# Kernel tuning notes

Hardware: AMD Instinct MI355X
Metric: run time of the kernel (lower is better)

The kernel has to match this reference:

```python
import jax, jax.numpy as jnp
import numpy as np

NUM_LAYERS = 3


def setup_inputs() -> dict:
    key = jax.random.key(0)
    k1, k2 = jax.random.split(key)
    N = 200000          # num_users + num_items
    D = 64              # latent_dim
    E = 4000000         # number of directed edges
    edge_index = jax.random.randint(k1, (2, E), 0, N, dtype=jnp.int64)
    emb_weight = 0.1 * jax.random.normal(k2, (N, D), dtype=jnp.float32)  # nn.init.normal_(std=0.1)
    return {"edge_index": edge_index, "emb_weight": emb_weight}


def reference(edge_index, emb_weight):
    N, D = emb_weight.shape
    src, dst = edge_index[0], edge_index[1]
    # gcn_norm (no self loops), as used by LGConv
    deg = jax.ops.segment_sum(jnp.ones_like(src, dtype=emb_weight.dtype), dst, num_segments=N)
    dinv = jnp.where(deg > 0, jax.lax.rsqrt(jnp.maximum(deg, 1.0)), 0.0)
    norm = dinv[src] * dinv[dst]            # [E]
    emb0 = emb_weight
    emb = emb0
    acc = emb0                              # running sum over layer embeddings
    for _ in range(NUM_LAYERS):
        msgs = norm[:, None] * emb[src]     # [E, D] irregular gather
        emb = jax.ops.segment_sum(msgs, dst, num_segments=N)  # scatter-add aggregate
        acc = acc + emb
    out = acc / (NUM_LAYERS + 1)            # mean over stacked layer embeddings
    return (emb0, out)
```

## Files before the change

### kernel.cpp

```cpp
#include <hip/hip_runtime.h>

#define DIM 64
#define BNODE_SHIFT 9
#define BNODE (1 << BNODE_SHIFT)
#define MAXNB 512
#define BIN_CHUNK 8192

__device__ inline float bf2f(unsigned int h) {
    return __uint_as_float((h & 0xFFFFu) << 16);
}
__device__ inline unsigned int f2bf2(float a, float b) {
    unsigned int ua = __float_as_uint(a);
    unsigned int ub = __float_as_uint(b);
    ua = (ua + 0x7FFFu + ((ua >> 16) & 1u)) >> 16;
    ub = (ub + 0x7FFFu + ((ub >> 16) & 1u)) >> 16;
    return ua | (ub << 16);
}

__global__ void hist_kernel(const int* __restrict__ dst, int* __restrict__ bucket_count,
                            int E, int NB) {
    __shared__ int h[MAXNB];
    const int t = threadIdx.x;
    for (int i = t; i < MAXNB; i += blockDim.x) h[i] = 0;
    __syncthreads();
    const long long beg = (long long)blockIdx.x * BIN_CHUNK;
    for (int j = 0; j < BIN_CHUNK / 256; ++j) {
        long long idx = beg + j * 256 + t;
        if (idx < E) atomicAdd(&h[dst[idx] >> BNODE_SHIFT], 1);
    }
    __syncthreads();
    for (int b = t; b < NB; b += blockDim.x)
        if (h[b]) atomicAdd(&bucket_count[b], h[b]);
}

__global__ void __launch_bounds__(MAXNB) bucket_scan_kernel(
        const int* __restrict__ bucket_count, int* __restrict__ bucket_base,
        int* __restrict__ bucket_cursor, int NB) {
    __shared__ int s[MAXNB];
    const int t = threadIdx.x;
    int c = (t < NB) ? bucket_count[t] : 0;
    s[t] = c;
    __syncthreads();
    for (int off = 1; off < MAXNB; off <<= 1) {
        int v = s[t];
        int a = (t >= off) ? s[t - off] : 0;
        __syncthreads();
        s[t] = v + a;
        __syncthreads();
    }
    if (t < NB) {
        int excl = s[t] - c;
        bucket_base[t] = excl;
        bucket_cursor[t] = excl;
    }
    if (t == 0) bucket_base[NB] = s[MAXNB - 1];
}

__global__ void bin_kernel(const int* __restrict__ src, const int* __restrict__ dst,
                           int* __restrict__ bucket_cursor, unsigned int* __restrict__ packed,
                           int E, int NB) {
    __shared__ int lhist[MAXNB];
    __shared__ int lbase[MAXNB];
    const int t = threadIdx.x;
    for (int i = t; i < MAXNB; i += blockDim.x) lhist[i] = 0;
    __syncthreads();
    const long long beg = (long long)blockIdx.x * BIN_CHUNK;
    for (int j = 0; j < BIN_CHUNK / 256; ++j) {
        long long idx = beg + j * 256 + t;
        if (idx < E) atomicAdd(&lhist[dst[idx] >> BNODE_SHIFT], 1);
    }
    __syncthreads();
    for (int b = t; b < NB; b += blockDim.x) {
        int c = lhist[b];
        lbase[b] = c ? atomicAdd(&bucket_cursor[b], c) : 0;
    }
    __syncthreads();
    for (int i = t; i < MAXNB; i += blockDim.x) lhist[i] = 0;
    __syncthreads();
    for (int j = 0; j < BIN_CHUNK / 256; ++j) {
        long long idx = beg + j * 256 + t;
        if (idx < E) {
            int d = dst[idx];
            int b = d >> BNODE_SHIFT;
            int lpos = atomicAdd(&lhist[b], 1);
            packed[lbase[b] + lpos] =
                (unsigned int)src[idx] | ((unsigned int)(d & (BNODE - 1)) << 18);
        }
    }
}

__global__ void __launch_bounds__(BNODE) csr_kernel(
        const int* __restrict__ bucket_base, const unsigned int* __restrict__ packed,
        int* __restrict__ csr_src, float* __restrict__ dinv,
        int4* __restrict__ desc, int N) {
    __shared__ int hist[BNODE];
    __shared__ int s[BNODE];
    const int t = threadIdx.x;
    const int b = blockIdx.x;
    const int b0 = bucket_base[b];
    const int cnt = bucket_base[b + 1] - b0;
    hist[t] = 0;
    __syncthreads();
    for (int i = t; i < cnt; i += BNODE)
        atomicAdd(&hist[packed[b0 + i] >> 18], 1);
    __syncthreads();
    s[t] = hist[t];
    __syncthreads();
    for (int off = 1; off < BNODE; off <<= 1) {
        int v = s[t];
        int a = (t >= off) ? s[t - off] : 0;
        __syncthreads();
        s[t] = v + a;
        __syncthreads();
    }
    const int deg = hist[t];
    const int excl = s[t] - deg;
    const int myBeg = b0 + excl;
    const int node = (b << BNODE_SHIFT) + t;
    float di2 = 0.0f;
    if (node < N) {
        float fd = (float)deg;
        di2 = deg > 0 ? 1.0f / fd : 0.0f;
        dinv[node] = deg > 0 ? rsqrtf(fd) : 0.0f;
    }
    __syncthreads();
    s[t] = excl;
    __syncthreads();
    for (int i = t; i < cnt; i += BNODE) {
        unsigned int p = packed[b0 + i];
        int lpos = atomicAdd(&s[p >> 18], 1);
        csr_src[b0 + lpos] = (int)(p & 0x3FFFFu);
    }
    __syncthreads();
    const int bin = deg < (BNODE - 1) ? deg : (BNODE - 1);
    hist[t] = 0;
    __syncthreads();
    atomicAdd(&hist[bin], 1);
    __syncthreads();
    s[t] = hist[t];
    __syncthreads();
    for (int off = 1; off < BNODE; off <<= 1) {
        int v = s[t];
        int a = (t >= off) ? s[t - off] : 0;
        __syncthreads();
        s[t] = v + a;
        __syncthreads();
    }
    int tot = hist[t];
    __syncthreads();
    hist[t] = s[t] - tot;
    __syncthreads();
    int pos = atomicAdd(&hist[bin], 1);
    desc[(b << BNODE_SHIFT) + pos] =
        make_int4(myBeg, myBeg + deg, node < N ? node : 0x7FFFFFFF, __float_as_int(di2));
}

__global__ void conv0_kernel(const float* __restrict__ emb0, const float* __restrict__ dinv,
                             float* __restrict__ out_emb0, unsigned int* __restrict__ S0,
                             int n4) {
    int i = blockIdx.x * blockDim.x + threadIdx.x;
    if (i >= n4) return;
    float4 v = ((const float4*)emb0)[i];
    ((float4*)out_emb0)[i] = v;
    float w = dinv[i >> 4];
    uint2 o;
    o.x = f2bf2(w * v.x, w * v.y);
    o.y = f2bf2(w * v.z, w * v.w);
    ((uint2*)S0)[i] = o;
}

template<bool LAST>
__global__ void gather_kernel(const int4* __restrict__ desc,
                              const int* __restrict__ csr_src,
                              const unsigned int* __restrict__ S_in,
                              unsigned int* __restrict__ S_out,
                              const unsigned int* __restrict__ S1,
                              const float* __restrict__ emb0,
                              float* __restrict__ acc,
                              int N, int NG) {
    int tid = blockIdx.x * blockDim.x + threadIdx.x;
    int g = tid >> 3;
    int q = tid & 7;
    if (g >= NG) return;
    const int4 d = desc[g];
    const int node = d.z;
    if (node >= N) return;
    float r0 = 0.f, r1 = 0.f, r2 = 0.f, r3 = 0.f, r4 = 0.f, r5 = 0.f, r6 = 0.f, r7 = 0.f;
    for (int i = d.x; i < d.y; ++i) {
        int sIdx = csr_src[i];
        uint4 gg = *(const uint4*)(S_in + (size_t)sIdx * (DIM / 2) + q * 4);
        r0 += bf2f(gg.x);
        r1 += bf2f(gg.x >> 16);
        r2 += bf2f(gg.y);
        r3 += bf2f(gg.y >> 16);
        r4 += bf2f(gg.z);
        r5 += bf2f(gg.z >> 16);
        r6 += bf2f(gg.w);
        r7 += bf2f(gg.w >> 16);
    }
    const float di2 = __int_as_float(d.w);
    if (!LAST) {
        uint4 o;
        o.x = f2bf2(di2 * r0, di2 * r1);
        o.y = f2bf2(di2 * r2, di2 * r3);
        o.z = f2bf2(di2 * r4, di2 * r5);
        o.w = f2bf2(di2 * r6, di2 * r7);
        *(uint4*)(S_out + (size_t)node * (DIM / 2) + q * 4) = o;
    } else {
        float rs = di2 > 0.f ? rsqrtf(di2) : 0.f;
        float dv = sqrtf(di2);
        uint4 a1 = *(const uint4*)(S1   + (size_t)node * (DIM / 2) + q * 4);
        uint4 a2 = *(const uint4*)(S_in + (size_t)node * (DIM / 2) + q * 4);
        const float* e = emb0 + (size_t)node * DIM + q * 8;
        float4 e0 = *(const float4*)(e);
        float4 e1 = *(const float4*)(e + 4);
        float4 o0, o1;
        o0.x = 0.25f * (e0.x + rs * (bf2f(a1.x) + bf2f(a2.x)) + dv * r0);
        o0.y = 0.25f * (e0.y + rs * (bf2f(a1.x >> 16) + bf2f(a2.x >> 16)) + dv * r1);
        o0.z = 0.25f * (e0.z + rs * (bf2f(a1.y) + bf2f(a2.y)) + dv * r2);
        o0.w = 0.25f * (e0.w + rs * (bf2f(a1.y >> 16) + bf2f(a2.y >> 16)) + dv * r3);
        o1.x = 0.25f * (e1.x + rs * (bf2f(a1.z) + bf2f(a2.z)) + dv * r4);
        o1.y = 0.25f * (e1.y + rs * (bf2f(a1.z >> 16) + bf2f(a2.z >> 16)) + dv * r5);
        o1.z = 0.25f * (e1.z + rs * (bf2f(a1.w) + bf2f(a2.w)) + dv * r6);
        o1.w = 0.25f * (e1.w + rs * (bf2f(a1.w >> 16) + bf2f(a2.w >> 16)) + dv * r7);
        float* ap = acc + (size_t)node * DIM + q * 8;
        *(float4*)(ap) = o0;
        *(float4*)(ap + 4) = o1;
    }
}

static inline size_t align256(size_t x) { return (x + 255) & ~(size_t)255; }

extern "C" void kernel_launch(void* const* d_in, const int* in_sizes, int n_in,
                              void* d_out, int out_size, void* d_ws, size_t ws_size,
                              hipStream_t stream) {
    const int*   edge = (const int*)d_in[0];
    const float* emb0 = (const float*)d_in[1];
    const int E = in_sizes[0] / 2;
    const int N = in_sizes[1] / DIM;
    const int* src = edge;
    const int* dst = edge + E;
    const int NB = (N + BNODE - 1) >> BNODE_SHIFT;

    char* ws = (char*)d_ws;
    int* bucket_count  = (int*)ws;  ws += align256((size_t)(MAXNB + 1) * sizeof(int));
    int* bucket_base   = (int*)ws;  ws += align256((size_t)(MAXNB + 1) * sizeof(int));
    int* bucket_cursor = (int*)ws;  ws += align256((size_t)(MAXNB + 1) * sizeof(int));
    float* dinv        = (float*)ws; ws += align256((size_t)N * sizeof(float));
    int4* desc         = (int4*)ws; ws += align256((size_t)NB * BNODE * sizeof(int4));
    unsigned int* packed = (unsigned int*)ws; ws += align256((size_t)E * sizeof(int));
    int* csr_src       = (int*)ws;  ws += align256((size_t)E * sizeof(int));
    unsigned int* SX   = (unsigned int*)ws; ws += align256((size_t)N * (DIM / 2) * sizeof(unsigned int));
    unsigned int* SY   = (unsigned int*)ws; ws += align256((size_t)N * (DIM / 2) * sizeof(unsigned int));

    float* out_emb0 = (float*)d_out;
    float* acc      = out_emb0 + (size_t)N * DIM;

    const int blocks_e = (int)(((long long)E + BIN_CHUNK - 1) / BIN_CHUNK);
    const int n4 = N * DIM / 4;

    hipMemsetAsync(bucket_count, 0, (size_t)(MAXNB + 1) * sizeof(int), stream);
    hist_kernel<<<blocks_e, 256, 0, stream>>>(dst, bucket_count, E, NB);
    bucket_scan_kernel<<<1, MAXNB, 0, stream>>>(bucket_count, bucket_base, bucket_cursor, NB);
    bin_kernel<<<blocks_e, 256, 0, stream>>>(src, dst, bucket_cursor, packed, E, NB);
    csr_kernel<<<NB, BNODE, 0, stream>>>(bucket_base, packed, csr_src, dinv, desc, N);

    conv0_kernel<<<(n4 + 255) / 256, 256, 0, stream>>>(emb0, dinv, out_emb0, SX, n4);

    const int NG = NB * BNODE;
    const int ggrid = (NG * 8 + 255) / 256;
    gather_kernel<false><<<ggrid, 256, 0, stream>>>(desc, csr_src, SX, SY, nullptr, nullptr, nullptr, N, NG);
    gather_kernel<false><<<ggrid, 256, 0, stream>>>(desc, csr_src, SY, SX, nullptr, nullptr, nullptr, N, NG);
    gather_kernel<true><<<ggrid, 256, 0, stream>>>(desc, csr_src, SX, nullptr, SY, emb0, acc, N, NG);
}
```

Before: 608.1 us.

## Assign one wavefront per node in gather and drop degree-sorted descriptors

The gather kernels now map each node to a 64-lane wavefront. Eight edge groups of eight lanes each read rows in parallel, with two loads in flight per lane, and the partial sums are combined with xor shuffles. The degree-binning sort of node descriptors in the CSR kernel is removed, so descriptors are written directly by node index. This is meant to expose more memory-level parallelism per node and remove the load imbalance of one 8-lane group walking a whole edge list. The cost is eight times as many threads and shuffle-reduction overhead for low-degree nodes, where most lanes sit idle.

```diff
diff --git a/kernel.cpp b/kernel.cpp
--- a/kernel.cpp
+++ b/kernel.cpp
@@ -117,11 +117,11 @@
     const int excl = s[t] - deg;
     const int myBeg = b0 + excl;
     const int node = (b << BNODE_SHIFT) + t;
-    float di2 = 0.0f;
     if (node < N) {
         float fd = (float)deg;
-        di2 = deg > 0 ? 1.0f / fd : 0.0f;
+        float di2 = deg > 0 ? 1.0f / fd : 0.0f;
         dinv[node] = deg > 0 ? rsqrtf(fd) : 0.0f;
+        desc[node] = make_int4(myBeg, myBeg + deg, deg, __float_as_int(di2));
     }
     __syncthreads();
     s[t] = excl;
@@ -131,28 +131,6 @@
         int lpos = atomicAdd(&s[p >> 18], 1);
         csr_src[b0 + lpos] = (int)(p & 0x3FFFFu);
     }
-    __syncthreads();
-    const int bin = deg < (BNODE - 1) ? deg : (BNODE - 1);
-    hist[t] = 0;
-    __syncthreads();
-    atomicAdd(&hist[bin], 1);
-    __syncthreads();
-    s[t] = hist[t];
-    __syncthreads();
-    for (int off = 1; off < BNODE; off <<= 1) {
-        int v = s[t];
-        int a = (t >= off) ? s[t - off] : 0;
-        __syncthreads();
-        s[t] = v + a;
-        __syncthreads();
-    }
-    int tot = hist[t];
-    __syncthreads();
-    hist[t] = s[t] - tot;
-    __syncthreads();
-    int pos = atomicAdd(&hist[bin], 1);
-    desc[(b << BNODE_SHIFT) + pos] =
-        make_int4(myBeg, myBeg + deg, node < N ? node : 0x7FFFFFFF, __float_as_int(di2));
 }
 
 __global__ void conv0_kernel(const float* __restrict__ emb0, const float* __restrict__ dinv,
@@ -169,6 +147,13 @@
     ((uint2*)S0)[i] = o;
 }
 
+__device__ inline void acc8(float r[8], uint4 g) {
+    r[0] += bf2f(g.x); r[1] += bf2f(g.x >> 16);
+    r[2] += bf2f(g.y); r[3] += bf2f(g.y >> 16);
+    r[4] += bf2f(g.z); r[5] += bf2f(g.z >> 16);
+    r[6] += bf2f(g.w); r[7] += bf2f(g.w >> 16);
+}
+
 template<bool LAST>
 __global__ void gather_kernel(const int4* __restrict__ desc,
                               const int* __restrict__ csr_src,
@@ -177,53 +162,61 @@
                               const unsigned int* __restrict__ S1,
                               const float* __restrict__ emb0,
                               float* __restrict__ acc,
-                              int N, int NG) {
-    int tid = blockIdx.x * blockDim.x + threadIdx.x;
-    int g = tid >> 3;
-    int q = tid & 7;
-    if (g >= NG) return;
-    const int4 d = desc[g];
-    const int node = d.z;
+                              int N) {
+    const int node = (blockIdx.x * blockDim.x + threadIdx.x) >> 6;
     if (node >= N) return;
-    float r0 = 0.f, r1 = 0.f, r2 = 0.f, r3 = 0.f, r4 = 0.f, r5 = 0.f, r6 = 0.f, r7 = 0.f;
-    for (int i = d.x; i < d.y; ++i) {
-        int sIdx = csr_src[i];
-        uint4 gg = *(const uint4*)(S_in + (size_t)sIdx * (DIM / 2) + q * 4);
-        r0 += bf2f(gg.x);
-        r1 += bf2f(gg.x >> 16);
-        r2 += bf2f(gg.y);
-        r3 += bf2f(gg.y >> 16);
-        r4 += bf2f(gg.z);
-        r5 += bf2f(gg.z >> 16);
-        r6 += bf2f(gg.w);
-        r7 += bf2f(gg.w >> 16);
-    }
+    const int lane = threadIdx.x & 63;
+    const int eg = lane >> 3;
+    const int q  = lane & 7;
+    const int4 d = desc[node];
+    const int end = d.y;
+    float r[8] = {0.f, 0.f, 0.f, 0.f, 0.f, 0.f, 0.f, 0.f};
+    int i = d.x + eg;
+    for (; i + 8 < end; i += 16) {
+        int s0 = csr_src[i];
+        int s1 = csr_src[i + 8];
+        uint4 g0 = *(const uint4*)(S_in + (size_t)s0 * (DIM / 2) + q * 4);
+        uint4 g1 = *(const uint4*)(S_in + (size_t)s1 * (DIM / 2) + q * 4);
+        acc8(r, g0);
+        acc8(r, g1);
+    }
+    if (i < end) {
+        int s0 = csr_src[i];
+        uint4 g0 = *(const uint4*)(S_in + (size_t)s0 * (DIM / 2) + q * 4);
+        acc8(r, g0);
+    }
+    #pragma unroll
+    for (int m = 8; m < 64; m <<= 1) {
+        #pragma unroll
+        for (int j = 0; j < 8; ++j) r[j] += __shfl_xor(r[j], m, 64);
+    }
+    if (lane >= 8) return;
     const float di2 = __int_as_float(d.w);
     if (!LAST) {
         uint4 o;
-        o.x = f2bf2(di2 * r0, di2 * r1);
-        o.y = f2bf2(di2 * r2, di2 * r3);
-        o.z = f2bf2(di2 * r4, di2 * r5);
-        o.w = f2bf2(di2 * r6, di2 * r7);
-        *(uint4*)(S_out + (size_t)node * (DIM / 2) + q * 4) = o;
+        o.x = f2bf2(di2 * r[0], di2 * r[1]);
+        o.y = f2bf2(di2 * r[2], di2 * r[3]);
+        o.z = f2bf2(di2 * r[4], di2 * r[5]);
+        o.w = f2bf2(di2 * r[6], di2 * r[7]);
+        *(uint4*)(S_out + (size_t)node * (DIM / 2) + lane * 4) = o;
     } else {
         float rs = di2 > 0.f ? rsqrtf(di2) : 0.f;
         float dv = sqrtf(di2);
-        uint4 a1 = *(const uint4*)(S1   + (size_t)node * (DIM / 2) + q * 4);
-        uint4 a2 = *(const uint4*)(S_in + (size_t)node * (DIM / 2) + q * 4);
-        const float* e = emb0 + (size_t)node * DIM + q * 8;
+        uint4 a1 = *(const uint4*)(S1   + (size_t)node * (DIM / 2) + lane * 4);
+        uint4 a2 = *(const uint4*)(S_in + (size_t)node * (DIM / 2) + lane * 4);
+        const float* e = emb0 + (size_t)node * DIM + lane * 8;
         float4 e0 = *(const float4*)(e);
         float4 e1 = *(const float4*)(e + 4);
         float4 o0, o1;
-        o0.x = 0.25f * (e0.x + rs * (bf2f(a1.x) + bf2f(a2.x)) + dv * r0);
-        o0.y = 0.25f * (e0.y + rs * (bf2f(a1.x >> 16) + bf2f(a2.x >> 16)) + dv * r1);
-        o0.z = 0.25f * (e0.z + rs * (bf2f(a1.y) + bf2f(a2.y)) + dv * r2);
-        o0.w = 0.25f * (e0.w + rs * (bf2f(a1.y >> 16) + bf2f(a2.y >> 16)) + dv * r3);
-        o1.x = 0.25f * (e1.x + rs * (bf2f(a1.z) + bf2f(a2.z)) + dv * r4);
-        o1.y = 0.25f * (e1.y + rs * (bf2f(a1.z >> 16) + bf2f(a2.z >> 16)) + dv * r5);
-        o1.z = 0.25f * (e1.z + rs * (bf2f(a1.w) + bf2f(a2.w)) + dv * r6);
-        o1.w = 0.25f * (e1.w + rs * (bf2f(a1.w >> 16) + bf2f(a2.w >> 16)) + dv * r7);
-        float* ap = acc + (size_t)node * DIM + q * 8;
+        o0.x = 0.25f * (e0.x + rs * (bf2f(a1.x) + bf2f(a2.x)) + dv * r[0]);
+        o0.y = 0.25f * (e0.y + rs * (bf2f(a1.x >> 16) + bf2f(a2.x >> 16)) + dv * r[1]);
+        o0.z = 0.25f * (e0.z + rs * (bf2f(a1.y) + bf2f(a2.y)) + dv * r[2]);
+        o0.w = 0.25f * (e0.w + rs * (bf2f(a1.y >> 16) + bf2f(a2.y >> 16)) + dv * r[3]);
+        o1.x = 0.25f * (e1.x + rs * (bf2f(a1.z) + bf2f(a2.z)) + dv * r[4]);
+        o1.y = 0.25f * (e1.y + rs * (bf2f(a1.z >> 16) + bf2f(a2.z >> 16)) + dv * r[5]);
+        o1.z = 0.25f * (e1.z + rs * (bf2f(a1.w) + bf2f(a2.w)) + dv * r[6]);
+        o1.w = 0.25f * (e1.w + rs * (bf2f(a1.w >> 16) + bf2f(a2.w >> 16)) + dv * r[7]);
+        float* ap = acc + (size_t)node * DIM + lane * 8;
         *(float4*)(ap) = o0;
         *(float4*)(ap + 4) = o1;
     }
@@ -247,7 +240,7 @@
     int* bucket_base   = (int*)ws;  ws += align256((size_t)(MAXNB + 1) * sizeof(int));
     int* bucket_cursor = (int*)ws;  ws += align256((size_t)(MAXNB + 1) * sizeof(int));
     float* dinv        = (float*)ws; ws += align256((size_t)N * sizeof(float));
-    int4* desc         = (int4*)ws; ws += align256((size_t)NB * BNODE * sizeof(int4));
+    int4* desc         = (int4*)ws; ws += align256((size_t)N * sizeof(int4));
     unsigned int* packed = (unsigned int*)ws; ws += align256((size_t)E * sizeof(int));
     int* csr_src       = (int*)ws;  ws += align256((size_t)E * sizeof(int));
     unsigned int* SX   = (unsigned int*)ws; ws += align256((size_t)N * (DIM / 2) * sizeof(unsigned int));
@@ -267,9 +260,9 @@
 
     conv0_kernel<<<(n4 + 255) / 256, 256, 0, stream>>>(emb0, dinv, out_emb0, SX, n4);
 
-    const int NG = NB * BNODE;
-    const int ggrid = (NG * 8 + 255) / 256;
-    gather_kernel<false><<<ggrid, 256, 0, stream>>>(desc, csr_src, SX, SY, nullptr, nullptr, nullptr, N, NG);
-    gather_kernel<false><<<ggrid, 256, 0, stream>>>(desc, csr_src, SY, SX, nullptr, nullptr, nullptr, N, NG);
-    gather_kernel<true><<<ggrid, 256, 0, stream>>>(desc, csr_src, SX, nullptr, SY, emb0, acc, N, NG);
-}
+    const long long gthreads = (long long)N * 64;
+    const int ggrid = (int)((gthreads + 255) / 256);
+    gather_kernel<false><<<ggrid, 256, 0, stream>>>(desc, csr_src, SX, SY, nullptr, nullptr, nullptr, N);
+    gather_kernel<false><<<ggrid, 256, 0, stream>>>(desc, csr_src, SY, SX, nullptr, nullptr, nullptr, N);
+    gather_kernel<true><<<ggrid, 256, 0, stream>>>(desc, csr_src, SX, nullptr, SY, emb0, acc, N);
+}
```

Result: faster. 547.5 us (-10.0%).
